# Kernel tuning notes

Measured on AMD Instinct MI355X. Metric: run time of the kernel, lower is better.

## Reference

```python
import jax, jax.numpy as jnp
import numpy as np

N_NODES = 8192
IN_F = 256
OUT_F = 256
ALPHA = 0.2  # LeakyReLU negative slope


def setup_inputs() -> dict:
    key = jax.random.key(0)
    k1, k2, k3, k4 = jax.random.split(key, 4)
    X = jax.random.normal(k1, (N_NODES, IN_F), dtype=jnp.float32)
    A = jax.random.randint(k2, (N_NODES, N_NODES), 0, 2, dtype=jnp.int32)
    # torch nn.Linear weight layout: (out_features, in_features)
    W = jax.random.normal(k3, (OUT_F, IN_F), dtype=jnp.float32) * (1.0 / np.sqrt(IN_F))
    r = jax.random.normal(k4, (2 * OUT_F, 1), dtype=jnp.float32)
    return {"X": X, "A": A, "W": W, "r": r}


def reference(X, A, W, r):
    # Wh = X @ W^T  -> (N, F_out)
    Wh = X @ W.T
    # Split r so that cat([Wh_i, Wh_j]) @ r == Wh_i @ r_src + Wh_j @ r_dst
    F_out = Wh.shape[-1]
    r_src = r[:F_out, 0]   # (F,)
    r_dst = r[F_out:, 0]   # (F,)
    s_i = Wh @ r_src       # (N,)
    s_j = Wh @ r_dst       # (N,)
    e = s_i[:, None] + s_j[None, :]                      # (N, N)
    e = jnp.where(e >= 0, e, ALPHA * e)                  # LeakyReLU
    e = jnp.where(A == 0, -jnp.inf, e)                   # mask non-edges
    attention = jax.nn.softmax(e, axis=1)                # row-wise softmax
    output = attention @ Wh                              # (N, F_out)
    return jax.nn.gelu(output, approximate=False)        # torch F.gelu (exact)
```

## Files before the change

### kernel.cpp

```cpp
#include <hip/hip_runtime.h>
#include <hip/hip_bf16.h>

#define N_NODES 8192
#define NF      256
#define L2E     1.44269504088896341f

typedef __attribute__((ext_vector_type(8))) short short8;
typedef __attribute__((ext_vector_type(4))) short short4v;
typedef __attribute__((ext_vector_type(4))) float floatx4;
typedef __attribute__((ext_vector_type(16))) float floatx16;

static __device__ __forceinline__ float bf2f(short s) {
    return __uint_as_float(((unsigned)(unsigned short)s) << 16);
}
static __device__ __forceinline__ short f2bf_rn(float f) {
    unsigned u = __float_as_uint(f) + 0x8000u;
    return (short)(u >> 16);
}
struct bfpair { short hi, lo; };
static __device__ __forceinline__ bfpair split_bf(float x) {
    bfpair p;
    p.hi = f2bf_rn(x);
    p.lo = f2bf_rn(x - bf2f(p.hi));
    return p;
}
static __device__ __forceinline__ void async16(const void* g, void* l) {
    __builtin_amdgcn_global_load_lds(
        (const __attribute__((address_space(1))) unsigned*)g,
        (__attribute__((address_space(3))) unsigned*)l, 16, 0, 0);
}

__global__ __launch_bounds__(256) void kx_split(const float* __restrict__ W,
                                                short* __restrict__ Whi,
                                                short* __restrict__ Wlo) {
    #pragma unroll
    for (int e = 0; e < 4; ++e) {
        const int i = blockIdx.x * 1024 + e * 256 + threadIdx.x;
        bfpair p = split_bf(W[i]);
        Whi[i] = p.hi;
        Wlo[i] = p.lo;
    }
}

__global__ __launch_bounds__(512) void k1_gemm(const float* __restrict__ X,
                                               const short* __restrict__ Whi,
                                               const short* __restrict__ Wlo,
                                               const float* __restrict__ r,
                                               short* __restrict__ WhT,
                                               float* __restrict__ sp_src,
                                               float* __restrict__ sp_dst) {
    __shared__ float Xs[32 * 256];

    const int tid = threadIdx.x;
    const int w = tid >> 6, lane = tid & 63;
    const int q = lane >> 4, m = lane & 15;
    const int rh = w >> 2, cq = w & 3;
    const int i_base = blockIdx.x * 32;

    #pragma unroll
    for (int v = 0; v < 4; ++v) {
        const int rowv = w * 4 + v;
        const int c = lane ^ (rowv & 7);
        async16(X + (size_t)(i_base + rowv) * NF + c * 4, &Xs[rowv * 256]);
    }
    __syncthreads();

    floatx4 acc[4] = {};
    const int xrow = rh * 16 + m;
    const int r7 = xrow & 7;
    #pragma unroll
    for (int ks = 0; ks < 8; ++ks) {
        const int c0 = ks * 8 + q * 2;
        float4 f0 = *(const float4*)(&Xs[xrow * 256 + ((c0 ^ r7) * 4)]);
        float4 f1 = *(const float4*)(&Xs[xrow * 256 + (((c0 + 1) ^ r7) * 4)]);
        const float xsv[8] = {f0.x, f0.y, f0.z, f0.w, f1.x, f1.y, f1.z, f1.w};
        short8 xh, xl;
        #pragma unroll
        for (int c = 0; c < 8; ++c) {
            bfpair p = split_bf(xsv[c]);
            xh[c] = p.hi; xl[c] = p.lo;
        }
        #pragma unroll
        for (int nt = 0; nt < 4; ++nt) {
            const int n = cq * 64 + nt * 16 + m;
            short8 wh = *(const short8*)(Whi + n * NF + ks * 32 + q * 8);
            short8 wl = *(const short8*)(Wlo + n * NF + ks * 32 + q * 8);
            acc[nt] = __builtin_amdgcn_mfma_f32_16x16x32_bf16(xh, wh, acc[nt], 0, 0, 0);
            acc[nt] = __builtin_amdgcn_mfma_f32_16x16x32_bf16(xl, wh, acc[nt], 0, 0, 0);
            acc[nt] = __builtin_amdgcn_mfma_f32_16x16x32_bf16(xh, wl, acc[nt], 0, 0, 0);
        }
    }

    const int i0 = i_base + rh * 16 + q * 4;
    float vs[4] = {0.f, 0.f, 0.f, 0.f}, vd[4] = {0.f, 0.f, 0.f, 0.f};
    #pragma unroll
    for (int nt = 0; nt < 4; ++nt) {
        const int n = cq * 64 + nt * 16 + m;
        short4v v;
        #pragma unroll
        for (int r2 = 0; r2 < 4; ++r2) v[r2] = f2bf_rn(acc[nt][r2]);
        *(short4v*)(WhT + (size_t)n * N_NODES + i0) = v;
        const float rs = r[n], rd = r[NF + n];
        #pragma unroll
        for (int r2 = 0; r2 < 4; ++r2) {
            vs[r2] = fmaf(acc[nt][r2], rs, vs[r2]);
            vd[r2] = fmaf(acc[nt][r2], rd, vd[r2]);
        }
    }
    #pragma unroll
    for (int mask = 1; mask <= 8; mask <<= 1) {
        #pragma unroll
        for (int r2 = 0; r2 < 4; ++r2) {
            vs[r2] += __shfl_xor(vs[r2], mask);
            vd[r2] += __shfl_xor(vd[r2], mask);
        }
    }
    if (m == 0) {
        #pragma unroll
        for (int r2 = 0; r2 < 4; ++r2) {
            sp_src[cq * N_NODES + i0 + r2] = vs[r2];
            sp_dst[cq * N_NODES + i0 + r2] = vd[r2];
        }
    }
}

__global__ __launch_bounds__(256) void k2_sv(const float* __restrict__ sp_src,
                                             const float* __restrict__ sp_dst,
                                             float* __restrict__ s_src,
                                             float* __restrict__ s_dst,
                                             float* __restrict__ pmax) {
    __shared__ float red[256];
    const int tid = threadIdx.x;
    const int i = blockIdx.x * 256 + tid;
    float ss = 0.f, sd = 0.f;
    #pragma unroll
    for (int nb = 0; nb < 4; ++nb) {
        ss += sp_src[nb * N_NODES + i];
        sd += sp_dst[nb * N_NODES + i];
    }
    s_src[i] = ss;
    s_dst[i] = sd;
    red[tid] = sd;
    __syncthreads();
    for (int off = 128; off > 0; off >>= 1) {
        if (tid < off) red[tid] = fmaxf(red[tid], red[tid + off]);
        __syncthreads();
    }
    if (tid == 0) pmax[blockIdx.x] = red[0];
}

static __device__ __forceinline__ void pgroup(const int4 a, const floatx4 t,
                                              const float s_i, const float d_i,
                                              float* p) {
    const int av[4] = {a.x, a.y, a.z, a.w};
    #pragma unroll
    for (int c = 0; c < 4; ++c) {
        float sum = s_i + t[c];
        float lr  = fmaxf(sum, 0.2f * sum);
        float pp  = __builtin_amdgcn_exp2f(fmaf(lr, L2E, d_i));
        p[c] = (av[c] != 0) ? pp : 0.0f;
    }
}

__global__ __launch_bounds__(512, 4) void k4_attn(const int* __restrict__ Adj,
                                                  const short* __restrict__ WhT,
                                                  const float* __restrict__ s_dst,
                                                  const float* __restrict__ s_src,
                                                  const float* __restrict__ pmax,
                                                  float* __restrict__ nump,
                                                  float* __restrict__ denp) {
    __shared__ union {
        short B[256 * 128];
        float red[8 * 16 * 64];
    } sm;
    __shared__ float denred[4 * 32];

    const int tid = threadIdx.x;
    const int w = tid >> 6, lane = tid & 63;
    const int jq = w & 3, nh = w >> 2;
    const int l31 = lane & 31, lh = lane >> 5, l15 = lane & 15;
    const int ib = (int)blockIdx.x >> 1, jh = (int)blockIdx.x & 1;
    const int i0 = ib * 32;
    const int row = i0 + l31;
    const int jbase = jh * 4096;

    float M = pmax[0];
    #pragma unroll
    for (int b = 1; b < 32; ++b) M = fmaxf(M, pmax[b]);
    const float s_i = s_src[row];
    const float e0 = s_i + M;
    const float d_i = -fmaxf(e0, 0.2f * e0) * L2E;

    int voff[8];
    #pragma unroll
    for (int v = 0; v < 8; ++v) {
        const int n = w * 32 + v * 4 + (lane >> 4);
        const int c = l15 ^ (n & 15);
        voff[v] = n * N_NODES + c * 8;
    }
    const short* gBbase = WhT + jbase;

    const int slot0 = (jq * 4 + lh) ^ l15;
    const int slot1 = (jq * 4 + 2 + lh) ^ l15;
    const int nrow = nh * 128 + l31;
    const int boffA = nrow * 128 + slot0 * 8;
    const int boffB = nrow * 128 + slot1 * 8;

    const int* aPtr = Adj + (size_t)row * N_NODES + jbase + jq * 32 + lh * 8;
    const float* tPtr = s_dst + jbase + jq * 32 + lh * 8;

    floatx16 acc[4] = {};
    float den = 0.f;

    for (int s = 0; s < 32; ++s) {
        const int jo = s * 128;
        #pragma unroll
        for (int v = 0; v < 8; ++v)
            async16(gBbase + jo + voff[v], sm.B + (w * 32 + v * 4) * 128);
        __syncthreads();

        int4 a0 = *(const int4*)(aPtr + jo);
        int4 a1 = *(const int4*)(aPtr + jo + 4);
        int4 a2 = *(const int4*)(aPtr + jo + 16);
        int4 a3 = *(const int4*)(aPtr + jo + 20);
        floatx4 t0 = *(const floatx4*)(tPtr + jo);
        floatx4 t1 = *(const floatx4*)(tPtr + jo + 4);
        floatx4 t2 = *(const floatx4*)(tPtr + jo + 16);
        floatx4 t3 = *(const floatx4*)(tPtr + jo + 20);

        float p[16];
        pgroup(a0, t0, s_i, d_i, p);
        pgroup(a1, t1, s_i, d_i, p + 4);
        pgroup(a2, t2, s_i, d_i, p + 8);
        pgroup(a3, t3, s_i, d_i, p + 12);

        short8 af0, af1;
        #pragma unroll
        for (int c = 0; c < 8; ++c) { af0[c] = f2bf_rn(p[c]); af1[c] = f2bf_rn(p[8 + c]); }
        float ds = 0.f;
        #pragma unroll
        for (int c = 0; c < 16; ++c) ds += p[c];
        den += ds;

        #pragma unroll
        for (int nt = 0; nt < 4; ++nt) {
            short8 b0 = *(const short8*)(sm.B + boffA + nt * 4096);
            short8 b1 = *(const short8*)(sm.B + boffB + nt * 4096);
            acc[nt] = __builtin_amdgcn_mfma_f32_32x32x16_bf16(af0, b0, acc[nt], 0, 0, 0);
            acc[nt] = __builtin_amdgcn_mfma_f32_32x32x16_bf16(af1, b1, acc[nt], 0, 0, 0);
        }
        __syncthreads();
    }

    den += __shfl_xor(den, 32);
    if (w < 4 && lane < 32) denred[w * 32 + lane] = den;

    float* numq = nump + (size_t)jh * N_NODES * NF;
    #pragma unroll
    for (int nt = 0; nt < 4; ++nt) {
        #pragma unroll
        for (int rg = 0; rg < 16; ++rg)
            sm.red[(w * 16 + rg) * 64 + lane] = acc[nt][rg];
        __syncthreads();
        if (nt == 0 && tid < 32) {
            float d = denred[tid] + denred[32 + tid] + denred[64 + tid] + denred[96 + tid];
            denp[jh * N_NODES + i0 + tid] = d;
        }
        const int nh2 = w & 1;
        const int rb = (w >> 1) * 4;
        #pragma unroll
        for (int k = 0; k < 4; ++k) {
            const int rg = rb + k;
            float v = sm.red[((nh2 * 4 + 0) * 16 + rg) * 64 + lane]
                    + sm.red[((nh2 * 4 + 1) * 16 + rg) * 64 + lane]
                    + sm.red[((nh2 * 4 + 2) * 16 + rg) * 64 + lane]
                    + sm.red[((nh2 * 4 + 3) * 16 + rg) * 64 + lane];
            const int rrow = (rg & 3) + 8 * (rg >> 2) + 4 * lh;
            const int nn = nh2 * 128 + nt * 32 + l31;
            numq[(size_t)(i0 + rrow) * NF + nn] = v;
        }
        __syncthreads();
    }
}

__global__ __launch_bounds__(256) void k5_out(const float* __restrict__ nump,
                                              const float* __restrict__ denp,
                                              float* __restrict__ out) {
    const int idx = blockIdx.x * 256 + threadIdx.x;
    const int i = idx >> 8;
    float num = nump[idx] + nump[N_NODES * NF + idx];
    float den = denp[i] + denp[N_NODES + i];
    float x = num / fmaxf(den, 1e-30f);
    out[idx] = 0.5f * x * (1.0f + erff(x * 0.70710678118f));
}

extern "C" void kernel_launch(void* const* d_in, const int* in_sizes, int n_in,
                              void* d_out, int out_size, void* d_ws, size_t ws_size,
                              hipStream_t stream) {
    const float* X = (const float*)d_in[0];
    const int*   A = (const int*)d_in[1];
    const float* W = (const float*)d_in[2];
    const float* r = (const float*)d_in[3];
    float* out = (float*)d_out;

    char* wsp = (char*)d_ws;
    short* WhT    = (short*)wsp;                    wsp += (size_t)NF * N_NODES * 2;
    short* Whi    = (short*)wsp;                    wsp += NF * NF * 2;
    short* Wlo    = (short*)wsp;                    wsp += NF * NF * 2;
    float* sp_src = (float*)wsp;                    wsp += 4 * N_NODES * 4;
    float* sp_dst = (float*)wsp;                    wsp += 4 * N_NODES * 4;
    float* s_src  = (float*)wsp;                    wsp += N_NODES * 4;
    float* s_dst  = (float*)wsp;                    wsp += N_NODES * 4;
    float* pmax   = (float*)wsp;                    wsp += 32 * 4;
    float* denp   = (float*)wsp;                    wsp += 2 * N_NODES * 4;
    float* nump   = (float*)wsp;

    kx_split<<<64, 256, 0, stream>>>(W, Whi, Wlo);
    k1_gemm<<<256, 512, 0, stream>>>(X, Whi, Wlo, r, WhT, sp_src, sp_dst);
    k2_sv<<<32, 256, 0, stream>>>(sp_src, sp_dst, s_src, s_dst, pmax);
    k4_attn<<<512, 512, 0, stream>>>(A, WhT, s_dst, s_src, pmax, nump, denp);
    k5_out<<<N_NODES * NF / 256, 256, 0, stream>>>(nump, denp, out);
}
```

Baseline: 495.5 us.

## Double-buffer Wh tile in LDS and prefetch adjacency for next step

The attention kernel's K-loop now uses two 64-column LDS buffers for the WhT tile instead of one 128-column buffer. The next tile's async copy and the next adjacency loads are issued before computing on the current tile, so one barrier per iteration replaces two and loads overlap with MFMA work. The step size halves and the iteration count doubles, with a new XOR swizzle for the smaller tile. This adds per-iteration overhead and costs some MFMA density per barrier.

```diff
diff --git a/kernel.cpp b/kernel.cpp
--- a/kernel.cpp
+++ b/kernel.cpp
@@ -170,7 +170,7 @@
                                                   float* __restrict__ nump,
                                                   float* __restrict__ denp) {
     __shared__ union {
-        short B[256 * 128];
+        short B[2][256 * 64];
         float red[8 * 16 * 64];
     } sm;
     __shared__ float denred[4 * 32];
@@ -178,7 +178,7 @@
     const int tid = threadIdx.x;
     const int w = tid >> 6, lane = tid & 63;
     const int jq = w & 3, nh = w >> 2;
-    const int l31 = lane & 31, lh = lane >> 5, l15 = lane & 15;
+    const int l31 = lane & 31, lh = lane >> 5;
     const int ib = (int)blockIdx.x >> 1, jh = (int)blockIdx.x & 1;
     const int i0 = ib * 32;
     const int row = i0 + l31;
@@ -191,64 +191,71 @@
     const float e0 = s_i + M;
     const float d_i = -fmaxf(e0, 0.2f * e0) * L2E;
 
-    int voff[8];
-    #pragma unroll
-    for (int v = 0; v < 8; ++v) {
-        const int n = w * 32 + v * 4 + (lane >> 4);
-        const int c = l15 ^ (n & 15);
-        voff[v] = n * N_NODES + c * 8;
+    int voff[4];
+    #pragma unroll
+    for (int v = 0; v < 4; ++v) {
+        const int rown = w * 32 + v * 8 + (lane >> 3);
+        const int c = (lane & 7) ^ (rown & 7);
+        voff[v] = rown * N_NODES + c * 8;
     }
     const short* gBbase = WhT + jbase;
 
-    const int slot0 = (jq * 4 + lh) ^ l15;
-    const int slot1 = (jq * 4 + 2 + lh) ^ l15;
-    const int nrow = nh * 128 + l31;
-    const int boffA = nrow * 128 + slot0 * 8;
-    const int boffB = nrow * 128 + slot1 * 8;
-
-    const int* aPtr = Adj + (size_t)row * N_NODES + jbase + jq * 32 + lh * 8;
-    const float* tPtr = s_dst + jbase + jq * 32 + lh * 8;
+    const int g = jq * 2 + lh;
+    int boff[4];
+    #pragma unroll
+    for (int nt = 0; nt < 4; ++nt) {
+        const int n = nh * 128 + nt * 32 + l31;
+        boff[nt] = n * 64 + ((g ^ (l31 & 7)) * 8);
+    }
+
+    const int j0 = jq * 16 + lh * 8;
+    const int* aPtr = Adj + (size_t)row * N_NODES + jbase + j0;
+    const float* tPtr = s_dst + jbase + j0;
 
     floatx16 acc[4] = {};
     float den = 0.f;
 
-    for (int s = 0; s < 32; ++s) {
-        const int jo = s * 128;
-        #pragma unroll
-        for (int v = 0; v < 8; ++v)
-            async16(gBbase + jo + voff[v], sm.B + (w * 32 + v * 4) * 128);
-        __syncthreads();
-
-        int4 a0 = *(const int4*)(aPtr + jo);
-        int4 a1 = *(const int4*)(aPtr + jo + 4);
-        int4 a2 = *(const int4*)(aPtr + jo + 16);
-        int4 a3 = *(const int4*)(aPtr + jo + 20);
-        floatx4 t0 = *(const floatx4*)(tPtr + jo);
-        floatx4 t1 = *(const floatx4*)(tPtr + jo + 4);
-        floatx4 t2 = *(const floatx4*)(tPtr + jo + 16);
-        floatx4 t3 = *(const floatx4*)(tPtr + jo + 20);
-
-        float p[16];
+    #pragma unroll
+    for (int v = 0; v < 4; ++v)
+        async16(gBbase + voff[v], &sm.B[0][(w * 32 + v * 8) * 64]);
+    int4 a0 = *(const int4*)(aPtr);
+    int4 a1 = *(const int4*)(aPtr + 4);
+    __syncthreads();
+
+    for (int s = 0; s < 64; ++s) {
+        const short* Bc = sm.B[s & 1];
+        short* Bn = sm.B[(s & 1) ^ 1];
+
+        if (s < 63) {
+            const int jo = (s + 1) * 64;
+            #pragma unroll
+            for (int v = 0; v < 4; ++v)
+                async16(gBbase + jo + voff[v], Bn + (w * 32 + v * 8) * 64);
+        }
+        const int an = (s < 63) ? (s + 1) * 64 : s * 64;
+        int4 na0 = *(const int4*)(aPtr + an);
+        int4 na1 = *(const int4*)(aPtr + an + 4);
+        const float* tp = tPtr + s * 64;
+        floatx4 t0 = *(const floatx4*)(tp);
+        floatx4 t1 = *(const floatx4*)(tp + 4);
+
+        float p[8];
         pgroup(a0, t0, s_i, d_i, p);
         pgroup(a1, t1, s_i, d_i, p + 4);
-        pgroup(a2, t2, s_i, d_i, p + 8);
-        pgroup(a3, t3, s_i, d_i, p + 12);
-
-        short8 af0, af1;
-        #pragma unroll
-        for (int c = 0; c < 8; ++c) { af0[c] = f2bf_rn(p[c]); af1[c] = f2bf_rn(p[8 + c]); }
+
+        short8 af;
         float ds = 0.f;
         #pragma unroll
-        for (int c = 0; c < 16; ++c) ds += p[c];
+        for (int c = 0; c < 8; ++c) { af[c] = f2bf_rn(p[c]); ds += p[c]; }
         den += ds;
 
         #pragma unroll
         for (int nt = 0; nt < 4; ++nt) {
-            short8 b0 = *(const short8*)(sm.B + boffA + nt * 4096);
-            short8 b1 = *(const short8*)(sm.B + boffB + nt * 4096);
-            acc[nt] = __builtin_amdgcn_mfma_f32_32x32x16_bf16(af0, b0, acc[nt], 0, 0, 0);
-            acc[nt] = __builtin_amdgcn_mfma_f32_32x32x16_bf16(af1, b1, acc[nt], 0, 0, 0);
-        }
+            short8 b = *(const short8*)(Bc + boff[nt]);
+            acc[nt] = __builtin_amdgcn_mfma_f32_32x32x16_bf16(af, b, acc[nt], 0, 0, 0);
+        }
+        a0 = na0; a1 = na1;
+
         __syncthreads();
     }
 
```

Measured after the change: 488.2 us. About the same (-1.5%).
